# Optimization experiments

Measured on AMD Instinct MI355X. Metric: run time of the kernel, lower is better.

The kernel has to match this reference:

```python
import jax, jax.numpy as jnp
import numpy as np

D_IN = 1024
D_OUT = 1024
H = 16


def setup_inputs() -> dict:
    key = jax.random.key(0)
    ks = jax.random.split(key, 11)
    B, Tq, Tk = 2, 2048, 2048
    s = 1.0 / np.sqrt(D_IN)
    return {
        "q": jax.random.normal(ks[0], (B, Tq, D_IN), jnp.float32),
        "k": jax.random.normal(ks[1], (B, Tk, D_IN), jnp.float32),
        "v": jax.random.normal(ks[2], (B, Tk, D_IN), jnp.float32),
        "Wq": jax.random.uniform(ks[3], (D_IN, D_OUT), jnp.float32, -s, s),
        "bq": jax.random.uniform(ks[4], (D_OUT,), jnp.float32, -s, s),
        "Wk": jax.random.uniform(ks[5], (D_IN, D_OUT), jnp.float32, -s, s),
        "bk": jax.random.uniform(ks[6], (D_OUT,), jnp.float32, -s, s),
        "Wv": jax.random.uniform(ks[7], (D_IN, D_OUT), jnp.float32, -s, s),
        "bv": jax.random.uniform(ks[8], (D_OUT,), jnp.float32, -s, s),
        "Wo": jax.random.uniform(ks[9], (D_OUT, D_OUT), jnp.float32, -s, s),
        "bo": jax.random.uniform(ks[10], (D_OUT,), jnp.float32, -s, s),
    }


def reference(q, k, v, Wq, bq, Wk, bk, Wv, bv, Wo, bo):
    B, Tq, _ = q.shape
    Tk = k.shape[1]
    hd = D_OUT // H
    # QKV projections, split heads -> [B, H, T, hd]
    qh = (q @ Wq + bq).reshape(B, Tq, H, hd).transpose(0, 2, 1, 3)
    kh = (k @ Wk + bk).reshape(B, Tk, H, hd).transpose(0, 2, 1, 3)
    vh = (v @ Wv + bv).reshape(B, Tk, H, hd).transpose(0, 2, 1, 3)
    # scaled dot-product attention (scale uses key dim = head_dim)
    scores = jnp.einsum("bhqd,bhkd->bhqk", qh, kh) / jnp.sqrt(jnp.float32(hd))
    attn = jax.nn.softmax(scores, axis=-1)
    x = jnp.einsum("bhqk,bhkd->bhqd", attn, vh)
    x = x.transpose(0, 2, 1, 3).reshape(B, Tq, D_OUT)
    return x @ Wo + bo
```

## Files before the change

kernel.cpp:

```cpp
#include <hip/hip_runtime.h>
#include <hip/hip_bf16.h>

typedef __attribute__((ext_vector_type(8))) short short8;
typedef __attribute__((ext_vector_type(4))) float f32x4;

__device__ __forceinline__ unsigned short f2bf(float f) {
    __hip_bfloat16 h = __float2bfloat16(f);
    unsigned short u;
    __builtin_memcpy(&u, &h, 2);
    return u;
}

#define GLD16(gp, lp) __builtin_amdgcn_global_load_lds( \
    (const __attribute__((address_space(1))) void*)(gp), \
    (__attribute__((address_space(3))) void*)(lp), 16, 0, 0)

__global__ __launch_bounds__(256) void convert3(
    const float* __restrict__ q, const float* __restrict__ k, const float* __restrict__ v,
    unsigned short* __restrict__ qb, unsigned short* __restrict__ kb, unsigned short* __restrict__ vb)
{
    const float* src; unsigned short* dst;
    switch (blockIdx.y) { case 0: src = q; dst = qb; break;
                          case 1: src = k; dst = kb; break;
                          default: src = v; dst = vb; break; }
    size_t i = ((size_t)blockIdx.x * 256 + threadIdx.x) * 8;
    float4 x0 = *(const float4*)&src[i];
    float4 x1 = *(const float4*)&src[i + 4];
    union { unsigned short s[8]; uint4 u; } p;
    p.s[0] = f2bf(x0.x); p.s[1] = f2bf(x0.y); p.s[2] = f2bf(x0.z); p.s[3] = f2bf(x0.w);
    p.s[4] = f2bf(x1.x); p.s[5] = f2bf(x1.y); p.s[6] = f2bf(x1.z); p.s[7] = f2bf(x1.w);
    *(uint4*)&dst[i] = p.u;
}

__global__ __launch_bounds__(256) void transpose_w(
    const float* __restrict__ W0, const float* __restrict__ W1,
    const float* __restrict__ W2, const float* __restrict__ W3,
    unsigned short* __restrict__ T0, unsigned short* __restrict__ T1,
    unsigned short* __restrict__ T2, unsigned short* __restrict__ T3)
{
    __shared__ unsigned short Ts[64 * 72];
    const float* W;
    unsigned short* T;
    switch (blockIdx.z) {
        case 0: W = W0; T = T0; break;
        case 1: W = W1; T = T1; break;
        case 2: W = W2; T = T2; break;
        default: W = W3; T = T3; break;
    }
    int tid = threadIdx.x;
    int c = tid & 7, r = tid >> 3;
    int k0 = blockIdx.x * 64, n0 = blockIdx.y * 64;
    for (int i = 0; i < 64; i += 32) {
        const float* src = &W[(size_t)(k0 + r + i) * 1024 + n0 + c * 8];
        float4 x0 = *(const float4*)src;
        float4 x1 = *(const float4*)(src + 4);
        unsigned short* d = &Ts[(r + i) * 72 + c * 8];
        d[0] = f2bf(x0.x); d[1] = f2bf(x0.y); d[2] = f2bf(x0.z); d[3] = f2bf(x0.w);
        d[4] = f2bf(x1.x); d[5] = f2bf(x1.y); d[6] = f2bf(x1.z); d[7] = f2bf(x1.w);
    }
    __syncthreads();
    for (int i = 0; i < 64; i += 32) {
        union { unsigned short s[8]; uint4 v; } u;
        for (int j = 0; j < 8; j++) u.s[j] = Ts[(c * 8 + j) * 72 + (r + i)];
        *(uint4*)&T[(size_t)(n0 + r + i) * 1024 + k0 + c * 8] = u.v;
    }
}

__device__ __forceinline__ void gemm_core(
    const unsigned short* __restrict__ A, const unsigned short* __restrict__ BT,
    const float* __restrict__ bias, void* __restrict__ outv,
    int mode, float scale)
{
    const int K = 1024;
    __shared__ unsigned short As[128 * 32];
    __shared__ unsigned short Bs[128 * 32];
    int tid = threadIdx.x;
    int m0 = blockIdx.x * 128, n0 = blockIdx.y * 128;
    int lane = tid & 63, wave = tid >> 6;
    int lm = lane & 15, quad = lane >> 4;
    int wm = (wave >> 1) * 64, wn = (wave & 1) * 64;

    int lrow = lane >> 2, lcol = (lane & 3) * 8;
    const unsigned short* Ag = A + (size_t)(m0 + wave * 32 + lrow) * K + lcol;
    const unsigned short* Bg = BT + (size_t)(n0 + wave * 32 + lrow) * K + lcol;
    unsigned short* AsW0 = &As[(wave * 32) * 32];
    unsigned short* AsW1 = &As[(wave * 32 + 16) * 32];
    unsigned short* BsW0 = &Bs[(wave * 32) * 32];
    unsigned short* BsW1 = &Bs[(wave * 32 + 16) * 32];

    f32x4 acc[4][4];
    for (int i = 0; i < 4; i++)
        for (int j = 0; j < 4; j++)
            for (int r = 0; r < 4; r++) acc[i][j][r] = 0.0f;

    for (int kb = 0; kb < K; kb += 32) {
        GLD16(Ag, AsW0);
        GLD16(Ag + 16 * K, AsW1);
        GLD16(Bg, BsW0);
        GLD16(Bg + 16 * K, BsW1);
        Ag += 32; Bg += 32;
        __syncthreads();
        short8 a[4], b[4];
        for (int i = 0; i < 4; i++)
            a[i] = *(const short8*)&As[(wm + i * 16 + lm) * 32 + quad * 8];
        for (int j = 0; j < 4; j++)
            b[j] = *(const short8*)&Bs[(wn + j * 16 + lm) * 32 + quad * 8];
        for (int i = 0; i < 4; i++)
            for (int j = 0; j < 4; j++)
                acc[i][j] = __builtin_amdgcn_mfma_f32_16x16x32_bf16(a[i], b[j], acc[i][j], 0, 0, 0);
        __syncthreads();
    }

    for (int j = 0; j < 4; j++) {
        int col = n0 + wn + j * 16 + lm;
        float bv = bias[col];
        for (int i = 0; i < 4; i++) {
            int rowb = m0 + wm + i * 16 + quad * 4;
            if (mode == 0) {
                float* out32 = (float*)outv;
                for (int r = 0; r < 4; r++)
                    out32[(size_t)(rowb + r) * 1024 + col] = (acc[i][j][r] + bv) * scale;
            } else if (mode == 1) {
                unsigned short* out16 = (unsigned short*)outv;
                int h = col >> 6, d = col & 63;
                int bb = rowb >> 11, t = rowb & 2047;
                size_t base = (((size_t)(bb * 16 + h)) * 2048 + t) * 64 + d;
                for (int r = 0; r < 4; r++)
                    out16[base + (size_t)r * 64] = f2bf((acc[i][j][r] + bv) * scale);
            } else {
                unsigned short* out16 = (unsigned short*)outv;
                int h = col >> 6, d = col & 63;
                int bb = rowb >> 11, t = rowb & 2047;
                ushort4 pk;
                pk.x = f2bf((acc[i][j][0] + bv) * scale);
                pk.y = f2bf((acc[i][j][1] + bv) * scale);
                pk.z = f2bf((acc[i][j][2] + bv) * scale);
                pk.w = f2bf((acc[i][j][3] + bv) * scale);
                *(ushort4*)&out16[(((size_t)(bb * 16 + h)) * 64 + d) * 2048 + t] = pk;
            }
        }
    }
}

__global__ __launch_bounds__(256) void qkv_gemm(
    const unsigned short* __restrict__ qbf, const unsigned short* __restrict__ kbf,
    const unsigned short* __restrict__ vbf,
    const unsigned short* __restrict__ WqT, const unsigned short* __restrict__ WkT,
    const unsigned short* __restrict__ WvT,
    const float* __restrict__ bq, const float* __restrict__ bk, const float* __restrict__ bv,
    unsigned short* __restrict__ Qh, unsigned short* __restrict__ Kh,
    unsigned short* __restrict__ VhT)
{
    switch (blockIdx.z) {
        case 0:  gemm_core(qbf, WqT, bq, Qh,  1, 0.125f); break;
        case 1:  gemm_core(kbf, WkT, bk, Kh,  1, 1.0f);   break;
        default: gemm_core(vbf, WvT, bv, VhT, 2, 1.0f);   break;
    }
}

__global__ __launch_bounds__(256) void out_gemm(
    const unsigned short* __restrict__ X, const unsigned short* __restrict__ WoT,
    const float* __restrict__ bo, float* __restrict__ out)
{
    gemm_core(X, WoT, bo, out, 0, 1.0f);
}

__global__ __launch_bounds__(256) void attn_kernel(
    const unsigned short* __restrict__ Qh, const unsigned short* __restrict__ Kh,
    const unsigned short* __restrict__ VhT, unsigned short* __restrict__ X)
{
    __shared__ unsigned short Ks[2][64 * 64];
    __shared__ unsigned short Vt[2][64 * 64];
    __shared__ unsigned short Ps[4][16 * 72];

    int tid = threadIdx.x;
    int qb = blockIdx.x & 31, bh = blockIdx.x >> 5;
    int b = bh >> 4, h = bh & 15;
    int lane = tid & 63, wave = tid >> 6;
    int lm = lane & 15, quad = lane >> 4;

    const unsigned short* Kbase = Kh + (size_t)bh * 2048 * 64;
    const unsigned short* Vbase = VhT + (size_t)bh * 64 * 2048;

    int srow = wave * 8 + (lane >> 3);
    int schk = ((lane & 7) ^ ((lane >> 3) & 7)) * 8;
    int swz  = (lm & 7);

    int qrow = qb * 64 + wave * 16 + lm;
    const unsigned short* qptr = Qh + ((size_t)bh * 2048 + qrow) * 64;
    short8 qf0 = *(const short8*)&qptr[quad * 8];
    short8 qf1 = *(const short8*)&qptr[32 + quad * 8];

    f32x4 o[4];
    float l_r[4];
    for (int d = 0; d < 4; d++)
        for (int r = 0; r < 4; r++) o[d][r] = 0.0f;
    for (int r = 0; r < 4; r++) l_r[r] = 0.0f;

    unsigned short* Pw = &Ps[wave][0];
    int c0 = (quad ^ swz) * 8;
    int c1 = ((quad + 4) ^ swz) * 8;

    {
        GLD16(&Kbase[(size_t)srow * 64 + schk],               &Ks[0][(wave * 8) * 64]);
        GLD16(&Kbase[(size_t)(32 + srow) * 64 + schk],        &Ks[0][(32 + wave * 8) * 64]);
        GLD16(&Vbase[(size_t)srow * 2048 + schk],             &Vt[0][(wave * 8) * 64]);
        GLD16(&Vbase[(size_t)(32 + srow) * 2048 + schk],      &Vt[0][(32 + wave * 8) * 64]);
    }
    __syncthreads();

    for (int kt = 0; kt < 32; kt++) {
        int cur = kt & 1;
        if (kt < 31) {
            int k1 = (kt + 1) * 64;
            int nxt = cur ^ 1;
            GLD16(&Kbase[(size_t)(k1 + srow) * 64 + schk],        &Ks[nxt][(wave * 8) * 64]);
            GLD16(&Kbase[(size_t)(k1 + 32 + srow) * 64 + schk],   &Ks[nxt][(32 + wave * 8) * 64]);
            GLD16(&Vbase[(size_t)srow * 2048 + k1 + schk],        &Vt[nxt][(wave * 8) * 64]);
            GLD16(&Vbase[(size_t)(32 + srow) * 2048 + k1 + schk], &Vt[nxt][(32 + wave * 8) * 64]);
        }

        f32x4 s[4];
        for (int n = 0; n < 4; n++) {
            short8 kb0 = *(const short8*)&Ks[cur][(n * 16 + lm) * 64 + c0];
            short8 kb1 = *(const short8*)&Ks[cur][(n * 16 + lm) * 64 + c1];
            f32x4 z;
            z[0] = z[1] = z[2] = z[3] = 0.0f;
            z = __builtin_amdgcn_mfma_f32_16x16x32_bf16(qf0, kb0, z, 0, 0, 0);
            z = __builtin_amdgcn_mfma_f32_16x16x32_bf16(qf1, kb1, z, 0, 0, 0);
            s[n] = z;
        }

        for (int n = 0; n < 4; n++)
            for (int r = 0; r < 4; r++) {
                float p = __expf(s[n][r]);
                l_r[r] += p;
                Pw[(quad * 4 + r) * 72 + n * 16 + lm] = f2bf(p);
            }
        asm volatile("s_waitcnt lgkmcnt(0)" ::: "memory");
        short8 pf0 = *(const short8*)&Pw[lm * 72 + quad * 8];
        short8 pf1 = *(const short8*)&Pw[lm * 72 + 32 + quad * 8];

        for (int d = 0; d < 4; d++) {
            short8 vb0 = *(const short8*)&Vt[cur][(d * 16 + lm) * 64 + c0];
            short8 vb1 = *(const short8*)&Vt[cur][(d * 16 + lm) * 64 + c1];
            o[d] = __builtin_amdgcn_mfma_f32_16x16x32_bf16(pf0, vb0, o[d], 0, 0, 0);
            o[d] = __builtin_amdgcn_mfma_f32_16x16x32_bf16(pf1, vb1, o[d], 0, 0, 0);
        }
        __syncthreads();
    }

    float inv[4];
    for (int r = 0; r < 4; r++) {
        float t = l_r[r];
        for (int off = 1; off < 16; off <<= 1) t += __shfl_xor(t, off);
        inv[r] = 1.0f / t;
    }

    for (int d = 0; d < 4; d++)
        for (int r = 0; r < 4; r++) {
            int row = qb * 64 + wave * 16 + quad * 4 + r;
            X[((size_t)b * 2048 + row) * 1024 + h * 64 + d * 16 + lm] = f2bf(o[d][r] * inv[r]);
        }
}

extern "C" void kernel_launch(void* const* d_in, const int* in_sizes, int n_in,
                              void* d_out, int out_size, void* d_ws, size_t ws_size,
                              hipStream_t stream)
{
    const float* q  = (const float*)d_in[0];
    const float* k  = (const float*)d_in[1];
    const float* v  = (const float*)d_in[2];
    const float* Wq = (const float*)d_in[3];
    const float* bq = (const float*)d_in[4];
    const float* Wk = (const float*)d_in[5];
    const float* bk = (const float*)d_in[6];
    const float* Wv = (const float*)d_in[7];
    const float* bv = (const float*)d_in[8];
    const float* Wo = (const float*)d_in[9];
    const float* bo = (const float*)d_in[10];

    unsigned short* ws  = (unsigned short*)d_ws;
    const unsigned int M1 = 1u << 20;
    unsigned short* WqT = ws;
    unsigned short* WkT = ws + M1;
    unsigned short* WvT = ws + 2 * M1;
    unsigned short* WoT = ws + 3 * M1;
    unsigned short* qbf = ws + 4 * M1;
    unsigned short* kbf = ws + 8 * M1;
    unsigned short* vbf = ws + 12 * M1;
    unsigned short* Qh  = ws + 16 * M1;
    unsigned short* Kh  = ws + 4 * M1;
    unsigned short* VhT = ws + 8 * M1;
    unsigned short* X   = ws + 12 * M1;

    convert3<<<dim3(2048, 3), 256, 0, stream>>>(q, k, v, qbf, kbf, vbf);
    transpose_w<<<dim3(16, 16, 4), 256, 0, stream>>>(Wq, Wk, Wv, Wo, WqT, WkT, WvT, WoT);
    qkv_gemm<<<dim3(32, 8, 3), 256, 0, stream>>>(qbf, kbf, vbf, WqT, WkT, WvT,
                                                 bq, bk, bv, Qh, Kh, VhT);
    attn_kernel<<<dim3(1024), 256, 0, stream>>>(Qh, Kh, VhT, X);
    out_gemm<<<dim3(32, 8), 256, 0, stream>>>(X, WoT, bo, (float*)d_out);
}
```

Before: 257.4 us.

## Keep attention probabilities in registers via transposed QK^T and double-buffer GEMM tiles

The attention kernel now computes S^T (K as the A operand) so each lane's exp outputs directly form the A fragment of a 16x16x16 MFMA for P·V. This removes the per-wave LDS round trip for P and its waitcnt stall. Softmax uses exp2 with log2(e) folded into the Q scale. The GEMM core also gains double-buffered LDS staging so global loads overlap MFMA work, at the cost of doubled LDS per block. As before, there is no max subtraction.

```diff
diff --git a/kernel.cpp b/kernel.cpp
--- a/kernel.cpp
+++ b/kernel.cpp
@@ -2,6 +2,7 @@
 #include <hip/hip_bf16.h>
 
 typedef __attribute__((ext_vector_type(8))) short short8;
+typedef __attribute__((ext_vector_type(4))) short short4v;
 typedef __attribute__((ext_vector_type(4))) float f32x4;
 
 __device__ __forceinline__ unsigned short f2bf(float f) {
@@ -9,6 +10,12 @@
     unsigned short u;
     __builtin_memcpy(&u, &h, 2);
     return u;
+}
+__device__ __forceinline__ short4v pack4bf(float a, float b, float c, float d) {
+    union { unsigned u[2]; short4v s; } r;
+    r.u[0] = ((unsigned)f2bf(b) << 16) | f2bf(a);
+    r.u[1] = ((unsigned)f2bf(d) << 16) | f2bf(c);
+    return r.s;
 }
 
 #define GLD16(gp, lp) __builtin_amdgcn_global_load_lds( \
@@ -72,8 +79,8 @@
     int mode, float scale)
 {
     const int K = 1024;
-    __shared__ unsigned short As[128 * 32];
-    __shared__ unsigned short Bs[128 * 32];
+    __shared__ unsigned short As[2][128 * 32];
+    __shared__ unsigned short Bs[2][128 * 32];
     int tid = threadIdx.x;
     int m0 = blockIdx.x * 128, n0 = blockIdx.y * 128;
     int lane = tid & 63, wave = tid >> 6;
@@ -83,28 +90,34 @@
     int lrow = lane >> 2, lcol = (lane & 3) * 8;
     const unsigned short* Ag = A + (size_t)(m0 + wave * 32 + lrow) * K + lcol;
     const unsigned short* Bg = BT + (size_t)(n0 + wave * 32 + lrow) * K + lcol;
-    unsigned short* AsW0 = &As[(wave * 32) * 32];
-    unsigned short* AsW1 = &As[(wave * 32 + 16) * 32];
-    unsigned short* BsW0 = &Bs[(wave * 32) * 32];
-    unsigned short* BsW1 = &Bs[(wave * 32 + 16) * 32];
 
     f32x4 acc[4][4];
     for (int i = 0; i < 4; i++)
         for (int j = 0; j < 4; j++)
             for (int r = 0; r < 4; r++) acc[i][j][r] = 0.0f;
 
-    for (int kb = 0; kb < K; kb += 32) {
-        GLD16(Ag, AsW0);
-        GLD16(Ag + 16 * K, AsW1);
-        GLD16(Bg, BsW0);
-        GLD16(Bg + 16 * K, BsW1);
-        Ag += 32; Bg += 32;
-        __syncthreads();
+    GLD16(Ag,          &As[0][(wave * 32) * 32]);
+    GLD16(Ag + 16 * K, &As[0][(wave * 32 + 16) * 32]);
+    GLD16(Bg,          &Bs[0][(wave * 32) * 32]);
+    GLD16(Bg + 16 * K, &Bs[0][(wave * 32 + 16) * 32]);
+    __syncthreads();
+
+    for (int it = 0; it < 32; it++) {
+        int cur = it & 1;
+        if (it < 31) {
+            int nxt = cur ^ 1;
+            const unsigned short* Agn = Ag + (it + 1) * 32;
+            const unsigned short* Bgn = Bg + (it + 1) * 32;
+            GLD16(Agn,          &As[nxt][(wave * 32) * 32]);
+            GLD16(Agn + 16 * K, &As[nxt][(wave * 32 + 16) * 32]);
+            GLD16(Bgn,          &Bs[nxt][(wave * 32) * 32]);
+            GLD16(Bgn + 16 * K, &Bs[nxt][(wave * 32 + 16) * 32]);
+        }
         short8 a[4], b[4];
         for (int i = 0; i < 4; i++)
-            a[i] = *(const short8*)&As[(wm + i * 16 + lm) * 32 + quad * 8];
+            a[i] = *(const short8*)&As[cur][(wm + i * 16 + lm) * 32 + quad * 8];
         for (int j = 0; j < 4; j++)
-            b[j] = *(const short8*)&Bs[(wn + j * 16 + lm) * 32 + quad * 8];
+            b[j] = *(const short8*)&Bs[cur][(wn + j * 16 + lm) * 32 + quad * 8];
         for (int i = 0; i < 4; i++)
             for (int j = 0; j < 4; j++)
                 acc[i][j] = __builtin_amdgcn_mfma_f32_16x16x32_bf16(a[i], b[j], acc[i][j], 0, 0, 0);
@@ -152,9 +165,9 @@
     unsigned short* __restrict__ VhT)
 {
     switch (blockIdx.z) {
-        case 0:  gemm_core(qbf, WqT, bq, Qh,  1, 0.125f); break;
-        case 1:  gemm_core(kbf, WkT, bk, Kh,  1, 1.0f);   break;
-        default: gemm_core(vbf, WvT, bv, VhT, 2, 1.0f);   break;
+        case 0:  gemm_core(qbf, WqT, bq, Qh,  1, 0.18033688011f); break;
+        case 1:  gemm_core(kbf, WkT, bk, Kh,  1, 1.0f);           break;
+        default: gemm_core(vbf, WvT, bv, VhT, 2, 1.0f);           break;
     }
 }
 
@@ -171,7 +184,6 @@
 {
     __shared__ unsigned short Ks[2][64 * 64];
     __shared__ unsigned short Vt[2][64 * 64];
-    __shared__ unsigned short Ps[4][16 * 72];
 
     int tid = threadIdx.x;
     int qb = blockIdx.x & 31, bh = blockIdx.x >> 5;
@@ -184,7 +196,9 @@
 
     int srow = wave * 8 + (lane >> 3);
     int schk = ((lane & 7) ^ ((lane >> 3) & 7)) * 8;
-    int swz  = (lm & 7);
+    int swz  = lm & 7;
+    int c0 = (quad ^ swz) * 8;
+    int c1 = ((quad + 4) ^ swz) * 8;
 
     int qrow = qb * 64 + wave * 16 + lm;
     const unsigned short* qptr = Qh + ((size_t)bh * 2048 + qrow) * 64;
@@ -192,21 +206,14 @@
     short8 qf1 = *(const short8*)&qptr[32 + quad * 8];
 
     f32x4 o[4];
-    float l_r[4];
-    for (int d = 0; d < 4; d++)
-        for (int r = 0; r < 4; r++) o[d][r] = 0.0f;
-    for (int r = 0; r < 4; r++) l_r[r] = 0.0f;
-
-    unsigned short* Pw = &Ps[wave][0];
-    int c0 = (quad ^ swz) * 8;
-    int c1 = ((quad + 4) ^ swz) * 8;
-
-    {
-        GLD16(&Kbase[(size_t)srow * 64 + schk],               &Ks[0][(wave * 8) * 64]);
-        GLD16(&Kbase[(size_t)(32 + srow) * 64 + schk],        &Ks[0][(32 + wave * 8) * 64]);
-        GLD16(&Vbase[(size_t)srow * 2048 + schk],             &Vt[0][(wave * 8) * 64]);
-        GLD16(&Vbase[(size_t)(32 + srow) * 2048 + schk],      &Vt[0][(32 + wave * 8) * 64]);
-    }
+    for (int n = 0; n < 4; n++)
+        for (int r = 0; r < 4; r++) o[n][r] = 0.0f;
+    float l = 0.0f;
+
+    GLD16(&Kbase[(size_t)srow * 64 + schk],          &Ks[0][(wave * 8) * 64]);
+    GLD16(&Kbase[(size_t)(32 + srow) * 64 + schk],   &Ks[0][(32 + wave * 8) * 64]);
+    GLD16(&Vbase[(size_t)srow * 2048 + schk],        &Vt[0][(wave * 8) * 64]);
+    GLD16(&Vbase[(size_t)(32 + srow) * 2048 + schk], &Vt[0][(32 + wave * 8) * 64]);
     __syncthreads();
 
     for (int kt = 0; kt < 32; kt++) {
@@ -220,48 +227,44 @@
             GLD16(&Vbase[(size_t)(32 + srow) * 2048 + k1 + schk], &Vt[nxt][(32 + wave * 8) * 64]);
         }
 
-        f32x4 s[4];
-        for (int n = 0; n < 4; n++) {
-            short8 kb0 = *(const short8*)&Ks[cur][(n * 16 + lm) * 64 + c0];
-            short8 kb1 = *(const short8*)&Ks[cur][(n * 16 + lm) * 64 + c1];
+        short4v pa[4];
+        for (int t = 0; t < 4; t++) {
+            short8 ka0 = *(const short8*)&Ks[cur][(t * 16 + lm) * 64 + c0];
+            short8 ka1 = *(const short8*)&Ks[cur][(t * 16 + lm) * 64 + c1];
             f32x4 z;
             z[0] = z[1] = z[2] = z[3] = 0.0f;
-            z = __builtin_amdgcn_mfma_f32_16x16x32_bf16(qf0, kb0, z, 0, 0, 0);
-            z = __builtin_amdgcn_mfma_f32_16x16x32_bf16(qf1, kb1, z, 0, 0, 0);
-            s[n] = z;
-        }
-
+            z = __builtin_amdgcn_mfma_f32_16x16x32_bf16(ka0, qf0, z, 0, 0, 0);
+            z = __builtin_amdgcn_mfma_f32_16x16x32_bf16(ka1, qf1, z, 0, 0, 0);
+            float p0 = __builtin_amdgcn_exp2f(z[0]);
+            float p1 = __builtin_amdgcn_exp2f(z[1]);
+            float p2 = __builtin_amdgcn_exp2f(z[2]);
+            float p3 = __builtin_amdgcn_exp2f(z[3]);
+            l += (p0 + p1) + (p2 + p3);
+            pa[t] = pack4bf(p0, p1, p2, p3);
+        }
+
+        int wo = (quad & 1) * 4;
+        for (int n = 0; n < 4; n++) {
+            int rbase = (n * 16 + lm) * 64;
+            for (int t = 0; t < 4; t++) {
+                int chunk = t * 2 + (quad >> 1);
+                short4v vb = *(const short4v*)&Vt[cur][rbase + ((chunk ^ swz) * 8) + wo];
+                o[n] = __builtin_amdgcn_mfma_f32_16x16x16bf16_1k(pa[t], vb, o[n], 0, 0, 0);
+            }
+        }
+        __syncthreads();
+    }
+
+    l += __shfl_xor(l, 16);
+    l += __shfl_xor(l, 32);
+    float inv = 1.0f / l;
+
+    for (int r = 0; r < 4; r++) {
+        float invr = __shfl(inv, (lane & 48) | (quad * 4 + r));
+        int row = qb * 64 + wave * 16 + quad * 4 + r;
         for (int n = 0; n < 4; n++)
-            for (int r = 0; r < 4; r++) {
-                float p = __expf(s[n][r]);
-                l_r[r] += p;
-                Pw[(quad * 4 + r) * 72 + n * 16 + lm] = f2bf(p);
-            }
-        asm volatile("s_waitcnt lgkmcnt(0)" ::: "memory");
-        short8 pf0 = *(const short8*)&Pw[lm * 72 + quad * 8];
-        short8 pf1 = *(const short8*)&Pw[lm * 72 + 32 + quad * 8];
-
-        for (int d = 0; d < 4; d++) {
-            short8 vb0 = *(const short8*)&Vt[cur][(d * 16 + lm) * 64 + c0];
-            short8 vb1 = *(const short8*)&Vt[cur][(d * 16 + lm) * 64 + c1];
-            o[d] = __builtin_amdgcn_mfma_f32_16x16x32_bf16(pf0, vb0, o[d], 0, 0, 0);
-            o[d] = __builtin_amdgcn_mfma_f32_16x16x32_bf16(pf1, vb1, o[d], 0, 0, 0);
-        }
-        __syncthreads();
-    }
-
-    float inv[4];
-    for (int r = 0; r < 4; r++) {
-        float t = l_r[r];
-        for (int off = 1; off < 16; off <<= 1) t += __shfl_xor(t, off);
-        inv[r] = 1.0f / t;
-    }
-
-    for (int d = 0; d < 4; d++)
-        for (int r = 0; r < 4; r++) {
-            int row = qb * 64 + wave * 16 + quad * 4 + r;
-            X[((size_t)b * 2048 + row) * 1024 + h * 64 + d * 16 + lm] = f2bf(o[d][r] * inv[r]);
-        }
+            X[((size_t)b * 2048 + row) * 1024 + h * 64 + n * 16 + lm] = f2bf(o[n][r] * invr);
+    }
 }
 
 extern "C" void kernel_launch(void* const* d_in, const int* in_sizes, int n_in,
```

Result: faster. 247.7 us (-3.8%).
